# Kernel optimization log

Hardware: AMD Instinct MI355X
Metric: run time of the kernel (lower is better)

The kernel has to match this reference:

```python
import jax, jax.numpy as jnp
import numpy as np
from jax import lax

D_MODEL, D_INNER, D_STATE, DT_RANK, D_CONV = 512, 1024, 16, 32, 4
B, L = 4, 1024

def setup_inputs() -> dict:
    key = jax.random.key(0)
    ks = jax.random.split(key, 10)
    s = lambda k, shp, sc=0.02: jax.random.normal(k, shp, jnp.float32) * sc
    x = jax.random.normal(ks[0], (B, L, D_MODEL), jnp.float32)
    in_proj_w = s(ks[1], (2 * D_INNER, D_MODEL))
    conv_w = s(ks[2], (D_INNER, 1, D_CONV), 0.1)
    conv_b = jnp.zeros((D_INNER,), jnp.float32)
    x_proj_w = s(ks[3], (DT_RANK + 2 * D_STATE, D_INNER))
    dt_proj_w = s(ks[4], (D_INNER, DT_RANK), DT_RANK ** -0.5)
    dt_proj_b = s(ks[5], (D_INNER,), 0.1)
    # S4D-real init: A_log = log(1..d_state) per channel
    A_log = jnp.log(jnp.tile(jnp.arange(1, D_STATE + 1, dtype=jnp.float32), (D_INNER, 1)))
    D = jnp.ones((D_INNER,), jnp.float32)
    out_proj_w = s(ks[6], (D_MODEL, D_INNER))
    return dict(x=x, in_proj_w=in_proj_w, conv_w=conv_w, conv_b=conv_b,
                x_proj_w=x_proj_w, dt_proj_w=dt_proj_w, dt_proj_b=dt_proj_b,
                A_log=A_log, D=D, out_proj_w=out_proj_w)

def _mamba_fwd(x, in_proj_w, conv_w, conv_b, x_proj_w, dt_proj_w, dt_proj_b, A_log, D, out_proj_w):
    # in_proj and split into ssm branch / gate branch
    xz = jnp.einsum('bld,ed->ble', x, in_proj_w)          # [B,L,2*d_inner]
    xc, z = jnp.split(xz, 2, axis=-1)
    # depthwise causal conv1d along L (torch pads d_conv-1 both sides then slices [:L])
    xt = jnp.transpose(xc, (0, 2, 1))                      # [B,d_inner,L]
    xt = lax.conv_general_dilated(xt, conv_w, (1,), [(D_CONV - 1, 0)],
                                  feature_group_count=D_INNER,
                                  dimension_numbers=('NCH', 'OIH', 'NCH'))
    xc = jnp.transpose(xt + conv_b[None, :, None], (0, 2, 1))  # [B,L,d_inner]
    xc = jax.nn.silu(xc)
    # input-dependent SSM params
    dbc = jnp.einsum('bld,ed->ble', xc, x_proj_w)          # [B,L,dt_rank+2*d_state]
    dt, Bm, Cm = jnp.split(dbc, [DT_RANK, DT_RANK + D_STATE], axis=-1)
    delta = jax.nn.softplus(jnp.einsum('blr,dr->bld', dt, dt_proj_w) + dt_proj_b)  # [B,L,d_inner]
    A = -jnp.exp(A_log)                                    # [d_inner,d_state]
    deltaA = jnp.exp(delta[..., None] * A)                 # [B,L,d_inner,d_state]
    deltaBx = delta[..., None] * Bm[:, :, None, :] * xc[..., None]
    # parallel (associative) scan: h_t = deltaA_t * h_{t-1} + deltaBx_t
    def combine(c1, c2):
        a1, b1 = c1
        a2, b2 = c2
        return a2 * a1, a2 * b1 + b2
    _, h = lax.associative_scan(combine, (deltaA, deltaBx), axis=1)
    y = jnp.sum(h * Cm[:, :, None, :], axis=-1) + D * xc   # [B,L,d_inner]
    y = y * jax.nn.silu(z)
    return jnp.einsum('bld,ed->ble', y, out_proj_w)        # [B,L,d_model]

def reference(x, in_proj_w, conv_w, conv_b, x_proj_w, dt_proj_w, dt_proj_b, A_log, D, out_proj_w):
    return _mamba_fwd(x, in_proj_w, conv_w, conv_b, x_proj_w, dt_proj_w, dt_proj_b, A_log, D, out_proj_w)
```

## Files before the change

### kernel.cpp

```cpp
#include <hip/hip_runtime.h>
#include <cstddef>
#include <cstdint>

#define DMODEL 512
#define DINNER 1024
#define DSTATE 16
#define DTRANK 32
#define DCONV  4
#define NB     4
#define NL     1024
#define NR     (NB * NL)
#define CH     32
#define NCHUNK (NL / CH)
#define LOG2E  1.4426950408889634f
#define LN2    0.6931471805599453f

typedef __attribute__((ext_vector_type(8))) short bf16x8;
typedef __attribute__((ext_vector_type(4))) float f32x4;

__device__ __forceinline__ unsigned short f2bf(float f) {
    unsigned u = __builtin_bit_cast(unsigned, f);
    unsigned r = u + 0x7FFFu + ((u >> 16) & 1u);
    return (unsigned short)(r >> 16);
}
__device__ __forceinline__ float bf2f(unsigned short h) {
    return __builtin_bit_cast(float, (unsigned)h << 16);
}

__device__ __forceinline__ void gload_lds16(const unsigned short* g, unsigned short* lds) {
    __builtin_amdgcn_global_load_lds(
        (const __attribute__((address_space(1))) void*)g,
        (__attribute__((address_space(3))) void*)lds, 16, 0, 0);
}

__global__ __launch_bounds__(256) void cast_all_kernel(
    const float* __restrict__ x, const float* __restrict__ w_in,
    const float* __restrict__ w_out, const float* __restrict__ w_xp,
    unsigned short* __restrict__ xh, unsigned short* __restrict__ wih,
    unsigned short* __restrict__ woh, unsigned short* __restrict__ xpwh)
{
    int i = blockIdx.x * 256 + threadIdx.x;
    const float* src; unsigned short* dst;
    if (i < 524288)       { src = x;     dst = xh;   }
    else if (i < 786432)  { src = w_in;  dst = wih;  i -= 524288; }
    else if (i < 917504)  { src = w_out; dst = woh;  i -= 786432; }
    else if (i < 933888)  { src = w_xp;  dst = xpwh; i -= 917504; }
    else return;
    float4 v = ((const float4*)src)[i];
    ushort4 o;
    o.x = f2bf(v.x); o.y = f2bf(v.y); o.z = f2bf(v.z); o.w = f2bf(v.w);
    ((ushort4*)dst)[i] = o;
}

template<int BN, int OUTBF>
__global__ __launch_bounds__(256) void gemm_bf16_kernel(
    const unsigned short* __restrict__ A, const unsigned short* __restrict__ Bw,
    void* __restrict__ Cv, int M, int N, int K)
{
    constexpr int BK = 64;
    constexpr int NFRAG = BN / 32;
    constexpr int BINSTR = BN / 32;
    __shared__ unsigned short As[128 * BK];
    __shared__ unsigned short Bs[BN * BK];

    const int tid  = threadIdx.x;
    const int lane = tid & 63;
    const int w    = tid >> 6;
    const int wm   = w >> 1, wn = w & 1;
    const int brow = blockIdx.y * 128;
    const int bcol = blockIdx.x * BN;

    const int srcslot = (lane & 7) ^ (lane >> 3);
    const unsigned short* ag[4];
    unsigned short* al[4];
#pragma unroll
    for (int i = 0; i < 4; ++i) {
        const int r = w * 32 + i * 8 + (lane >> 3);
        ag[i] = A + (size_t)(brow + r) * K + srcslot * 8;
        al[i] = As + (w * 256 + i * 64) * 8;
    }
    const unsigned short* bg[BINSTR];
    unsigned short* bl[BINSTR];
#pragma unroll
    for (int i = 0; i < BINSTR; ++i) {
        const int r = w * 8 * BINSTR + i * 8 + (lane >> 3);
        bg[i] = Bw + (size_t)(bcol + r) * K + srcslot * 8;
        bl[i] = Bs + (w * 64 * BINSTR + i * 64) * 8;
    }

    const int fr = lane & 15;
    const int fq = lane >> 4;
    f32x4 acc[4][NFRAG] = {};

    for (int k0 = 0; k0 < K; k0 += BK) {
#pragma unroll
        for (int i = 0; i < 4; ++i) gload_lds16(ag[i] + k0, al[i]);
#pragma unroll
        for (int i = 0; i < BINSTR; ++i) gload_lds16(bg[i] + k0, bl[i]);
        __syncthreads();
#pragma unroll
        for (int ks = 0; ks < 2; ++ks) {
            bf16x8 af[4], bfr[NFRAG];
#pragma unroll
            for (int m = 0; m < 4; ++m) {
                const int r = wm * 64 + m * 16 + fr;
                const int s = (ks * 4 + fq) ^ (r & 7);
                af[m] = *(const bf16x8*)(As + r * BK + s * 8);
            }
#pragma unroll
            for (int n = 0; n < NFRAG; ++n) {
                const int r = wn * (BN / 2) + n * 16 + fr;
                const int s = (ks * 4 + fq) ^ (r & 7);
                bfr[n] = *(const bf16x8*)(Bs + r * BK + s * 8);
            }
#pragma unroll
            for (int m = 0; m < 4; ++m)
#pragma unroll
                for (int n = 0; n < NFRAG; ++n)
                    acc[m][n] = __builtin_amdgcn_mfma_f32_16x16x32_bf16(
                        af[m], bfr[n], acc[m][n], 0, 0, 0);
        }
        __syncthreads();
    }

    const int row0 = brow + wm * 64;
    const int col0 = bcol + wn * (BN / 2);
#pragma unroll
    for (int m = 0; m < 4; ++m)
#pragma unroll
        for (int n = 0; n < NFRAG; ++n)
#pragma unroll
            for (int j = 0; j < 4; ++j) {
                const size_t ci = (size_t)(row0 + m * 16 + fq * 4 + j) * N + col0 + n * 16 + fr;
                if (OUTBF) ((unsigned short*)Cv)[ci] = f2bf(acc[m][n][j]);
                else       ((float*)Cv)[ci] = acc[m][n][j];
            }
}

__global__ __launch_bounds__(256) void conv_silu_kernel(
    const unsigned short* __restrict__ xzh, const float* __restrict__ conv_w,
    const float* __restrict__ conv_b, unsigned short* __restrict__ xch)
{
    const int idx4 = blockIdx.x * 256 + threadIdx.x;
    const int e4 = idx4 & (DINNER / 4 - 1);
    const int r  = idx4 >> 8;
    const int l  = r & (NL - 1);
    const float4 cb = ((const float4*)conv_b)[e4];
    float4 w[4];
#pragma unroll
    for (int c = 0; c < 4; ++c) w[c] = ((const float4*)conv_w)[e4 * 4 + c];
    const ushort4 uz = {0, 0, 0, 0};
    const ushort4 u0 = (l >= 3) ? ((const ushort4*)(xzh + (size_t)(r - 3) * 2 * DINNER))[e4] : uz;
    const ushort4 u1 = (l >= 2) ? ((const ushort4*)(xzh + (size_t)(r - 2) * 2 * DINNER))[e4] : uz;
    const ushort4 u2 = (l >= 1) ? ((const ushort4*)(xzh + (size_t)(r - 1) * 2 * DINNER))[e4] : uz;
    const ushort4 u3 = ((const ushort4*)(xzh + (size_t)r * 2 * DINNER))[e4];
    float4 o;
    o.x = cb.x + w[0].x * bf2f(u0.x) + w[0].y * bf2f(u1.x) + w[0].z * bf2f(u2.x) + w[0].w * bf2f(u3.x);
    o.y = cb.y + w[1].x * bf2f(u0.y) + w[1].y * bf2f(u1.y) + w[1].z * bf2f(u2.y) + w[1].w * bf2f(u3.y);
    o.z = cb.z + w[2].x * bf2f(u0.z) + w[2].y * bf2f(u1.z) + w[2].z * bf2f(u2.z) + w[2].w * bf2f(u3.z);
    o.w = cb.w + w[3].x * bf2f(u0.w) + w[3].y * bf2f(u1.w) + w[3].z * bf2f(u2.w) + w[3].w * bf2f(u3.w);
    float4 s;
    s.x = o.x * __builtin_amdgcn_rcpf(1.f + __builtin_amdgcn_exp2f(-o.x * LOG2E));
    s.y = o.y * __builtin_amdgcn_rcpf(1.f + __builtin_amdgcn_exp2f(-o.y * LOG2E));
    s.z = o.z * __builtin_amdgcn_rcpf(1.f + __builtin_amdgcn_exp2f(-o.z * LOG2E));
    s.w = o.w * __builtin_amdgcn_rcpf(1.f + __builtin_amdgcn_exp2f(-o.w * LOG2E));
    ushort4 h4;
    h4.x = f2bf(s.x); h4.y = f2bf(s.y); h4.z = f2bf(s.z); h4.w = f2bf(s.w);
    ((ushort4*)xch)[idx4] = h4;
}

#define DRT 32
__global__ __launch_bounds__(256) void delta_kernel(
    const float* __restrict__ dbc, const float* __restrict__ dtw,
    const float* __restrict__ dtb, float* __restrict__ delta)
{
    __shared__ float dlds[DRT * DTRANK];
    const int t = threadIdx.x;
    const int e = blockIdx.x * 256 + t;
    const int r0 = blockIdx.y * DRT;
    for (int i = t; i < DRT * DTRANK; i += 256) {
        const int row = i >> 5, jj = i & 31;
        dlds[i] = dbc[(size_t)(r0 + row) * 64 + jj];
    }
    float4 wv[8];
    const float4* dtw4 = (const float4*)(dtw + (size_t)e * DTRANK);
#pragma unroll
    for (int q = 0; q < 8; ++q) wv[q] = dtw4[q];
    const float bias = dtb[e];
    __syncthreads();
#pragma unroll 4
    for (int row = 0; row < DRT; ++row) {
        const float4* dl4 = (const float4*)(dlds + row * DTRANK);
        float sum = bias;
#pragma unroll
        for (int q = 0; q < 8; ++q) {
            const float4 dv = dl4[q];
            const float4 w = wv[q];
            sum += dv.x * w.x + dv.y * w.y + dv.z * w.z + dv.w * w.w;
        }
        const float u = __builtin_amdgcn_exp2f(-fabsf(sum) * LOG2E);
        delta[(size_t)(r0 + row) * DINNER + e] =
            fmaxf(sum, 0.f) + __builtin_amdgcn_logf(1.f + u) * LN2;
    }
}

__global__ __launch_bounds__(256) void scanA_kernel(
    const float* __restrict__ delta, const unsigned short* __restrict__ xch,
    const float* __restrict__ dbc, const float* __restrict__ A_log,
    float* __restrict__ chunkP, float* __restrict__ chunkS)
{
    const int tid = threadIdx.x;
    const int e = blockIdx.x * 256 + tid;
    const int b = blockIdx.y, ck = blockIdx.z;
    const int rbase = b * NL + ck * CH;

    float Aes2[DSTATE];
    const float4* al4 = (const float4*)(A_log + (size_t)e * DSTATE);
#pragma unroll
    for (int q = 0; q < 4; ++q) {
        const float4 a = al4[q];
        Aes2[q * 4 + 0] = -__expf(a.x) * LOG2E;
        Aes2[q * 4 + 1] = -__expf(a.y) * LOG2E;
        Aes2[q * 4 + 2] = -__expf(a.z) * LOG2E;
        Aes2[q * 4 + 3] = -__expf(a.w) * LOG2E;
    }

    float S[DSTATE];
#pragma unroll
    for (int s = 0; s < DSTATE; ++s) S[s] = 0.f;
    float cum = 0.f;
    const float* dp = delta + (size_t)rbase * DINNER + e;
    const unsigned short* xp = xch + (size_t)rbase * DINNER + e;
    for (int l = 0; l < CH; ++l) {
        const float dl = dp[(size_t)l * DINNER];
        const float xv = bf2f(xp[(size_t)l * DINNER]);
        const float* bu = dbc + (size_t)(rbase + l) * 64 + DTRANK;
        cum += dl;
        const float common = dl * xv;
#pragma unroll
        for (int s = 0; s < DSTATE; ++s) {
            const float dA = __builtin_amdgcn_exp2f(dl * Aes2[s]);
            S[s] = fmaf(dA, S[s], common * bu[s]);
        }
    }
    const size_t oi = (((size_t)b * NCHUNK + ck) * DINNER + e) * DSTATE;
    float4* Pp = (float4*)(chunkP + oi);
    float4* Sp = (float4*)(chunkS + oi);
#pragma unroll
    for (int q = 0; q < 4; ++q) {
        float4 pv, sv;
        pv.x = __builtin_amdgcn_exp2f(cum * Aes2[q * 4 + 0]);
        pv.y = __builtin_amdgcn_exp2f(cum * Aes2[q * 4 + 1]);
        pv.z = __builtin_amdgcn_exp2f(cum * Aes2[q * 4 + 2]);
        pv.w = __builtin_amdgcn_exp2f(cum * Aes2[q * 4 + 3]);
        sv.x = S[q * 4 + 0]; sv.y = S[q * 4 + 1];
        sv.z = S[q * 4 + 2]; sv.w = S[q * 4 + 3];
        Pp[q] = pv; Sp[q] = sv;
    }
}

__global__ __launch_bounds__(256) void scanB_kernel(
    const float* __restrict__ chunkP, float* __restrict__ chunkS)
{
    const int idx = blockIdx.x * 256 + threadIdx.x;
    const int b = idx >> 14;
    const int rem = idx & (DINNER * DSTATE - 1);
    const size_t base = (size_t)b * NCHUNK * (DINNER * DSTATE) + rem;
    float P[NCHUNK], S[NCHUNK];
#pragma unroll
    for (int c = 0; c < NCHUNK; ++c) {
        P[c] = chunkP[base + (size_t)c * (DINNER * DSTATE)];
        S[c] = chunkS[base + (size_t)c * (DINNER * DSTATE)];
    }
    float h = 0.f;
#pragma unroll
    for (int c = 0; c < NCHUNK; ++c) {
        chunkS[base + (size_t)c * (DINNER * DSTATE)] = h;
        h = fmaf(P[c], h, S[c]);
    }
}

__global__ __launch_bounds__(256) void scanC_kernel(
    const unsigned short* __restrict__ xzh, const unsigned short* __restrict__ xch,
    const float* __restrict__ dbc, const float* __restrict__ A_log,
    const float* __restrict__ Dp, const float* __restrict__ hinit,
    const float* __restrict__ delta, unsigned short* __restrict__ yh)
{
    const int tid = threadIdx.x;
    const int e = blockIdx.x * 256 + tid;
    const int b = blockIdx.y, ck = blockIdx.z;
    const int rbase = b * NL + ck * CH;

    float Aes2[DSTATE];
    const float4* al4 = (const float4*)(A_log + (size_t)e * DSTATE);
#pragma unroll
    for (int q = 0; q < 4; ++q) {
        const float4 a = al4[q];
        Aes2[q * 4 + 0] = -__expf(a.x) * LOG2E;
        Aes2[q * 4 + 1] = -__expf(a.y) * LOG2E;
        Aes2[q * 4 + 2] = -__expf(a.z) * LOG2E;
        Aes2[q * 4 + 3] = -__expf(a.w) * LOG2E;
    }

    float h[DSTATE];
    const size_t oi = (((size_t)b * NCHUNK + ck) * DINNER + e) * DSTATE;
    const float4* h4 = (const float4*)(hinit + oi);
#pragma unroll
    for (int q = 0; q < 4; ++q) {
        const float4 v = h4[q];
        h[q * 4 + 0] = v.x; h[q * 4 + 1] = v.y; h[q * 4 + 2] = v.z; h[q * 4 + 3] = v.w;
    }
    const float Dv = Dp[e];

    const float* dp = delta + (size_t)rbase * DINNER + e;
    const unsigned short* xp = xch + (size_t)rbase * DINNER + e;
    const unsigned short* zp = xzh + (size_t)rbase * (2 * DINNER) + DINNER + e;
    unsigned short* yp = yh + (size_t)rbase * DINNER + e;

    for (int l = 0; l < CH; ++l) {
        const float dl = dp[(size_t)l * DINNER];
        const float xv = bf2f(xp[(size_t)l * DINNER]);
        const float zv = bf2f(zp[(size_t)l * 2 * DINNER]);
        const float* bu = dbc + (size_t)(rbase + l) * 64 + DTRANK;
        const float common = dl * xv;
        float y = 0.f;
#pragma unroll
        for (int s = 0; s < DSTATE; ++s) {
            const float dA = __builtin_amdgcn_exp2f(dl * Aes2[s]);
            h[s] = fmaf(dA, h[s], common * bu[s]);
            y = fmaf(h[s], bu[DSTATE + s], y);
        }
        y = fmaf(Dv, xv, y);
        const float sig = __builtin_amdgcn_rcpf(1.f + __builtin_amdgcn_exp2f(-zv * LOG2E));
        yp[(size_t)l * DINNER] = f2bf(y * (zv * sig));
    }
}

extern "C" void kernel_launch(void* const* d_in, const int* in_sizes, int n_in,
                              void* d_out, int out_size, void* d_ws, size_t ws_size,
                              hipStream_t stream)
{
    const float* x          = (const float*)d_in[0];
    const float* in_proj_w  = (const float*)d_in[1];
    const float* conv_w     = (const float*)d_in[2];
    const float* conv_b     = (const float*)d_in[3];
    const float* x_proj_w   = (const float*)d_in[4];
    const float* dt_proj_w  = (const float*)d_in[5];
    const float* dt_proj_b  = (const float*)d_in[6];
    const float* A_log      = (const float*)d_in[7];
    const float* Dp         = (const float*)d_in[8];
    const float* out_proj_w = (const float*)d_in[9];
    float* out = (float*)d_out;

    float* ws     = (float*)d_ws;
    float* dbc    = ws;
    float* yb     = dbc + (size_t)NR * 64;
    float* chunkS = yb + (size_t)NR * DINNER;
    float* chunkP = chunkS + (size_t)NB * NCHUNK * DINNER * DSTATE;
    unsigned short* xzh  = (unsigned short*)(chunkP + (size_t)NB * NCHUNK * DINNER * DSTATE);
    unsigned short* xch  = xzh + (size_t)NR * 2 * DINNER;
    unsigned short* yh   = xch + (size_t)NR * DINNER;
    unsigned short* xh   = yh + (size_t)NR * DINNER;
    unsigned short* wih  = xh + (size_t)NR * DMODEL;
    unsigned short* woh  = wih + (size_t)2 * DINNER * DMODEL;
    unsigned short* xpwh = woh + (size_t)DMODEL * DINNER;

    cast_all_kernel<<<(933888 + 255) / 256, 256, 0, stream>>>(
        x, in_proj_w, out_proj_w, x_proj_w, xh, wih, woh, xpwh);

    gemm_bf16_kernel<128, 1><<<dim3(2 * DINNER / 128, NR / 128), 256, 0, stream>>>(
        xh, wih, xzh, NR, 2 * DINNER, DMODEL);
    conv_silu_kernel<<<NR * DINNER / 1024, 256, 0, stream>>>(xzh, conv_w, conv_b, xch);
    gemm_bf16_kernel<64, 0><<<dim3(1, NR / 128), 256, 0, stream>>>(
        xch, xpwh, dbc, NR, 64, DINNER);
    delta_kernel<<<dim3(DINNER / 256, NR / DRT), 256, 0, stream>>>(
        dbc, dt_proj_w, dt_proj_b, yb);
    scanA_kernel<<<dim3(DINNER / 256, NB, NCHUNK), 256, 0, stream>>>(
        yb, xch, dbc, A_log, chunkP, chunkS);
    scanB_kernel<<<NB * DINNER * DSTATE / 256, 256, 0, stream>>>(chunkP, chunkS);
    scanC_kernel<<<dim3(DINNER / 256, NB, NCHUNK), 256, 0, stream>>>(
        xzh, xch, dbc, A_log, Dp, chunkS, yb, yh);
    gemm_bf16_kernel<64, 0><<<dim3(DMODEL / 64, NR / 128), 256, 0, stream>>>(
        yh, woh, out, NR, DMODEL, DINNER);
}
```

Before: 133.7 us.

## Split-K the x_proj GEMM with atomics and stream the chunk-state scan

Replaces the x_proj GEMM, which launched only 32 blocks, with a split-K kernel that runs 4 K-slices per row tile and accumulates into dbc with float atomics. The cast kernel now also zeroes dbc so the atomics start from zero. The intent is to fill more compute units on a small-N, large-K GEMM. The chunk-state scan kernel now loads and stores one chunk at a time instead of buffering all chunks in registers, which lowers register pressure. The LDS destination addressing is also rewritten into an equivalent form, and the atomic accumulation makes the summation order nondeterministic.

```diff
diff --git a/kernel.cpp b/kernel.cpp
--- a/kernel.cpp
+++ b/kernel.cpp
@@ -6,7 +6,6 @@
 #define DINNER 1024
 #define DSTATE 16
 #define DTRANK 32
-#define DCONV  4
 #define NB     4
 #define NL     1024
 #define NR     (NB * NL)
@@ -37,15 +36,23 @@
     const float* __restrict__ x, const float* __restrict__ w_in,
     const float* __restrict__ w_out, const float* __restrict__ w_xp,
     unsigned short* __restrict__ xh, unsigned short* __restrict__ wih,
-    unsigned short* __restrict__ woh, unsigned short* __restrict__ xpwh)
+    unsigned short* __restrict__ woh, unsigned short* __restrict__ xpwh,
+    float* __restrict__ dbc)
 {
     int i = blockIdx.x * 256 + threadIdx.x;
+    if (i >= 933888) {
+        i -= 933888;
+        if (i < 65536) {
+            const float4 z = {0.f, 0.f, 0.f, 0.f};
+            ((float4*)dbc)[i] = z;
+        }
+        return;
+    }
     const float* src; unsigned short* dst;
     if (i < 524288)       { src = x;     dst = xh;   }
     else if (i < 786432)  { src = w_in;  dst = wih;  i -= 524288; }
     else if (i < 917504)  { src = w_out; dst = woh;  i -= 786432; }
-    else if (i < 933888)  { src = w_xp;  dst = xpwh; i -= 917504; }
-    else return;
+    else                  { src = w_xp;  dst = xpwh; i -= 917504; }
     float4 v = ((const float4*)src)[i];
     ushort4 o;
     o.x = f2bf(v.x); o.y = f2bf(v.y); o.z = f2bf(v.z); o.w = f2bf(v.w);
@@ -77,7 +84,7 @@
     for (int i = 0; i < 4; ++i) {
         const int r = w * 32 + i * 8 + (lane >> 3);
         ag[i] = A + (size_t)(brow + r) * K + srcslot * 8;
-        al[i] = As + (w * 256 + i * 64) * 8;
+        al[i] = As + (w * 32 + i * 8) * BK;
     }
     const unsigned short* bg[BINSTR];
     unsigned short* bl[BINSTR];
@@ -85,7 +92,7 @@
     for (int i = 0; i < BINSTR; ++i) {
         const int r = w * 8 * BINSTR + i * 8 + (lane >> 3);
         bg[i] = Bw + (size_t)(bcol + r) * K + srcslot * 8;
-        bl[i] = Bs + (w * 64 * BINSTR + i * 64) * 8;
+        bl[i] = Bs + (w * 8 * BINSTR + i * 8) * BK;
     }
 
     const int fr = lane & 15;
@@ -135,6 +142,88 @@
                 if (OUTBF) ((unsigned short*)Cv)[ci] = f2bf(acc[m][n][j]);
                 else       ((float*)Cv)[ci] = acc[m][n][j];
             }
+}
+
+#define KS 4
+__global__ __launch_bounds__(256) void xproj_splitk_kernel(
+    const unsigned short* __restrict__ A, const unsigned short* __restrict__ Bw,
+    float* __restrict__ dbc, int K)
+{
+    constexpr int BK = 64;
+    __shared__ unsigned short As[128 * BK];
+    __shared__ unsigned short Bs[64 * BK];
+
+    const int tid  = threadIdx.x;
+    const int lane = tid & 63;
+    const int w    = tid >> 6;
+    const int wm   = w >> 1, wn = w & 1;
+    const int brow = blockIdx.x * 128;
+    const int kbase = blockIdx.y * (K / KS);
+
+    const int srcslot = (lane & 7) ^ (lane >> 3);
+    const unsigned short* ag[4];
+    unsigned short* al[4];
+#pragma unroll
+    for (int i = 0; i < 4; ++i) {
+        const int r = w * 32 + i * 8 + (lane >> 3);
+        ag[i] = A + (size_t)(brow + r) * K + kbase + srcslot * 8;
+        al[i] = As + (w * 32 + i * 8) * BK;
+    }
+    const unsigned short* bg[2];
+    unsigned short* bl[2];
+#pragma unroll
+    for (int i = 0; i < 2; ++i) {
+        const int r = w * 16 + i * 8 + (lane >> 3);
+        bg[i] = Bw + (size_t)r * K + kbase + srcslot * 8;
+        bl[i] = Bs + (w * 16 + i * 8) * BK;
+    }
+
+    const int fr = lane & 15;
+    const int fq = lane >> 4;
+    f32x4 acc[4][2] = {};
+
+    for (int k0 = 0; k0 < K / KS; k0 += BK) {
+#pragma unroll
+        for (int i = 0; i < 4; ++i) gload_lds16(ag[i] + k0, al[i]);
+#pragma unroll
+        for (int i = 0; i < 2; ++i) gload_lds16(bg[i] + k0, bl[i]);
+        __syncthreads();
+#pragma unroll
+        for (int ks = 0; ks < 2; ++ks) {
+            bf16x8 af[4], bfr[2];
+#pragma unroll
+            for (int m = 0; m < 4; ++m) {
+                const int r = wm * 64 + m * 16 + fr;
+                const int s = (ks * 4 + fq) ^ (r & 7);
+                af[m] = *(const bf16x8*)(As + r * BK + s * 8);
+            }
+#pragma unroll
+            for (int n = 0; n < 2; ++n) {
+                const int r = wn * 32 + n * 16 + fr;
+                const int s = (ks * 4 + fq) ^ (r & 7);
+                bfr[n] = *(const bf16x8*)(Bs + r * BK + s * 8);
+            }
+#pragma unroll
+            for (int m = 0; m < 4; ++m)
+#pragma unroll
+                for (int n = 0; n < 2; ++n)
+                    acc[m][n] = __builtin_amdgcn_mfma_f32_16x16x32_bf16(
+                        af[m], bfr[n], acc[m][n], 0, 0, 0);
+        }
+        __syncthreads();
+    }
+
+    const int row0 = brow + wm * 64;
+    const int col0 = wn * 32;
+#pragma unroll
+    for (int m = 0; m < 4; ++m)
+#pragma unroll
+        for (int n = 0; n < 2; ++n)
+#pragma unroll
+            for (int j = 0; j < 4; ++j)
+                unsafeAtomicAdd(
+                    &dbc[(size_t)(row0 + m * 16 + fq * 4 + j) * 64 + col0 + n * 16 + fr],
+                    acc[m][n][j]);
 }
 
 __global__ __launch_bounds__(256) void conv_silu_kernel(
@@ -266,17 +355,14 @@
     const int b = idx >> 14;
     const int rem = idx & (DINNER * DSTATE - 1);
     const size_t base = (size_t)b * NCHUNK * (DINNER * DSTATE) + rem;
-    float P[NCHUNK], S[NCHUNK];
-#pragma unroll
+    float h = 0.f;
+#pragma unroll 8
     for (int c = 0; c < NCHUNK; ++c) {
-        P[c] = chunkP[base + (size_t)c * (DINNER * DSTATE)];
-        S[c] = chunkS[base + (size_t)c * (DINNER * DSTATE)];
-    }
-    float h = 0.f;
-#pragma unroll
-    for (int c = 0; c < NCHUNK; ++c) {
-        chunkS[base + (size_t)c * (DINNER * DSTATE)] = h;
-        h = fmaf(P[c], h, S[c]);
+        const size_t i = base + (size_t)c * (DINNER * DSTATE);
+        const float P = chunkP[i];
+        const float S = chunkS[i];
+        chunkS[i] = h;
+        h = fmaf(P, h, S);
     }
 }
 
@@ -365,14 +451,14 @@
     unsigned short* woh  = wih + (size_t)2 * DINNER * DMODEL;
     unsigned short* xpwh = woh + (size_t)DMODEL * DINNER;
 
-    cast_all_kernel<<<(933888 + 255) / 256, 256, 0, stream>>>(
-        x, in_proj_w, out_proj_w, x_proj_w, xh, wih, woh, xpwh);
+    cast_all_kernel<<<(999424 + 255) / 256, 256, 0, stream>>>(
+        x, in_proj_w, out_proj_w, x_proj_w, xh, wih, woh, xpwh, dbc);
 
     gemm_bf16_kernel<128, 1><<<dim3(2 * DINNER / 128, NR / 128), 256, 0, stream>>>(
         xh, wih, xzh, NR, 2 * DINNER, DMODEL);
     conv_silu_kernel<<<NR * DINNER / 1024, 256, 0, stream>>>(xzh, conv_w, conv_b, xch);
-    gemm_bf16_kernel<64, 0><<<dim3(1, NR / 128), 256, 0, stream>>>(
-        xch, xpwh, dbc, NR, 64, DINNER);
+    xproj_splitk_kernel<<<dim3(NR / 128, KS), 256, 0, stream>>>(
+        xch, xpwh, dbc, DINNER);
     delta_kernel<<<dim3(DINNER / 256, NR / DRT), 256, 0, stream>>>(
         dbc, dt_proj_w, dt_proj_b, yb);
     scanA_kernel<<<dim3(DINNER / 256, NB, NCHUNK), 256, 0, stream>>>(
```

Result: faster. 128.0 us (-4.3%).
